# Performance work log

Hardware: AMD Instinct MI355X
Metric: run time of the kernel (lower is better)

The kernel has to match this reference:

```python
import jax, jax.numpy as jnp
import numpy as np

D = 1024
H = 16
DH = D // H


def setup_inputs() -> dict:
    key = jax.random.key(0)
    ks = jax.random.split(key, 7)
    s = 0.02
    return {
        "z": jax.random.normal(ks[0], (8, 1024, D), dtype=jnp.float32),
        "ln_w": jnp.ones((D,), dtype=jnp.float32),
        "ln_b": jnp.zeros((D,), dtype=jnp.float32),
        "W_qkv": jax.random.normal(ks[1], (D, 3 * D), dtype=jnp.float32) * s,
        "b_qkv": jnp.zeros((3 * D,), dtype=jnp.float32),
        "W_proj": jax.random.normal(ks[2], (D, D), dtype=jnp.float32) * s,
        "b_proj": jnp.zeros((D,), dtype=jnp.float32),
    }


def reference(z, ln_w, ln_b, W_qkv, b_qkv, W_proj, b_proj):
    b, n, d = z.shape
    # Pre-LN
    mu = jnp.mean(z, axis=-1, keepdims=True)
    var = jnp.var(z, axis=-1, keepdims=True)
    zn = (z - mu) / jnp.sqrt(var + 1e-5) * ln_w + ln_b
    # QKV projection: [b, n, 3, H, DH]
    qkv = (zn @ W_qkv + b_qkv).reshape(b, n, 3, H, DH)
    q = qkv[:, :, 0].transpose(0, 2, 1, 3)  # [b, H, n, DH]
    k = qkv[:, :, 1].transpose(0, 2, 1, 3)
    v = qkv[:, :, 2].transpose(0, 2, 1, 3)
    scale = 1.0 / jnp.sqrt(jnp.asarray(DH, dtype=z.dtype))
    scores = jnp.einsum("bhqd,bhkd->bhqk", q, k) * scale
    attn = jax.nn.softmax(scores, axis=-1)
    msa = jnp.einsum("bhqk,bhkd->bhqd", attn, v)  # [b, H, n, DH]
    msa_cat = msa.transpose(0, 2, 1, 3).reshape(b, n, d)
    out = msa_cat @ W_proj + b_proj
    return z + out
```

## Files before the change

kernel.cpp:

```cpp
#include <hip/hip_runtime.h>
#include <stdint.h>

typedef unsigned short u16;
typedef uint8_t u8;
typedef __bf16 bf16x8 __attribute__((ext_vector_type(8)));
typedef float f32x4 __attribute__((ext_vector_type(4)));
typedef int i32x8 __attribute__((ext_vector_type(8)));

#define D_MODEL 1024
#define NHEADS  16
#define DHEAD   64
#define BATCH   8
#define SEQ     1024
#define MTOT    (BATCH*SEQ)

#define GPTR(p) ((const __attribute__((address_space(1))) void*)(p))
#define LPTR(p) ((__attribute__((address_space(3))) void*)(p))

#if defined(__HIP_DEVICE_COMPILE__)
  #define MFMA_FP8_16x16x128(a, b, c) \
      __builtin_amdgcn_mfma_scale_f32_16x16x128_f8f6f4((a), (b), (c), 0, 0, 0, 127, 0, 127)
  #define CVT_PK_FP8(a, b, old, w) __builtin_amdgcn_cvt_pk_fp8_f32((a), (b), (old), (w))
#else
  #define MFMA_FP8_16x16x128(a, b, c) (c)
  #define CVT_PK_FP8(a, b, old, w) (0)
#endif

__device__ __forceinline__ u16 f2bf(float f) {
    union { float f; uint32_t u; } v; v.f = f;
    uint32_t u = v.u;
    u += 0x7fffu + ((u >> 16) & 1u);
    return (u16)(u >> 16);
}

__device__ __forceinline__ uint32_t pklo(int i1, int i0) {
    return __builtin_amdgcn_perm((uint32_t)i1, (uint32_t)i0, 0x05040100u);
}

__global__ __launch_bounds__(256) void prep_inputs(
    const float* __restrict__ z, const float* __restrict__ w,
    const float* __restrict__ b, uint32_t* __restrict__ znf,
    const float* __restrict__ Wqkv, const float* __restrict__ Wproj,
    u8* __restrict__ outQkv, u8* __restrict__ outProj)
{
    __shared__ float red[8];
    __shared__ u8 tile[32][36];
    const int bid = blockIdx.x;
    const int t = threadIdx.x;
    if (bid < MTOT) {
        const int row = bid;
        const float4 v = reinterpret_cast<const float4*>(z + (size_t)row * D_MODEL)[t];
        float s  = v.x + v.y + v.z + v.w;
        float s2 = v.x*v.x + v.y*v.y + v.z*v.z + v.w*v.w;
        #pragma unroll
        for (int off = 32; off; off >>= 1) {
            s  += __shfl_down(s,  off, 64);
            s2 += __shfl_down(s2, off, 64);
        }
        const int wave = t >> 6, lane = t & 63;
        if (lane == 0) { red[wave] = s; red[wave + 4] = s2; }
        __syncthreads();
        if (t == 0) {
            float ts  = red[0] + red[1] + red[2] + red[3];
            float ts2 = red[4] + red[5] + red[6] + red[7];
            float mu  = ts * (1.0f / D_MODEL);
            float var = ts2 * (1.0f / D_MODEL) - mu * mu;
            red[0] = mu; red[1] = rsqrtf(var + 1e-5f);
        }
        __syncthreads();
        const float mu = red[0], rstd = red[1];
        const float4 wv = reinterpret_cast<const float4*>(w)[t];
        const float4 bv = reinterpret_cast<const float4*>(b)[t];
        const float x0 = (v.x - mu) * rstd * wv.x + bv.x;
        const float x1 = (v.y - mu) * rstd * wv.y + bv.y;
        const float x2 = (v.z - mu) * rstd * wv.z + bv.z;
        const float x3 = (v.w - mu) * rstd * wv.w + bv.w;
        int pk = CVT_PK_FP8(x0, x1, 0, false);
        pk = CVT_PK_FP8(x2, x3, pk, true);
        znf[(size_t)row * (D_MODEL / 4) + t] = (uint32_t)pk;
    } else {
        const int bx = bid - MTOT;
        const int cx = bx & 127;
        const int r0 = (bx >> 7) * 32;
        const float* in; u8* out; int C;
        if (cx < 96) { in = Wqkv;  out = outQkv;  C = 3072; }
        else         { in = Wproj; out = outProj; C = 1024; }
        const int c0 = (cx < 96 ? cx : cx - 96) * 32;
        const int tx = t & 31, ty = t >> 5;
        #pragma unroll
        for (int i = 0; i < 4; ++i) {
            const float f = in[(size_t)(r0 + ty + i*8) * C + c0 + tx];
            tile[ty + i*8][tx] = (u8)(CVT_PK_FP8(f, 0.f, 0, false) & 0xFF);
        }
        __syncthreads();
        #pragma unroll
        for (int i = 0; i < 4; ++i)
            out[(size_t)(c0 + ty + i*8) * D_MODEL + r0 + tx] = tile[tx][ty + i*8];
    }
}

#define QSCALE 23.0831207f

#define FP8_MAINLOOP(A_, Bt_, MFMA_STMT)                                        \
    __shared__ u8 As[128 * 128];                                                \
    __shared__ u8 Bs[128 * 128];                                                \
    const int tid = threadIdx.x;                                                \
    const int wave = tid >> 6, lane = tid & 63;                                 \
    const int lm = lane & 15, g = lane >> 4;                                    \
    const int wm = (wave >> 1) * 64, wn = (wave & 1) * 64;                      \
    const int m0 = blockIdx.y * 128, n0 = blockIdx.x * 128;                     \
    const int srow = tid >> 3;                                                  \
    const int sseg = tid & 7;                                                   \
    const int sgcol = (sseg ^ (srow & 7)) * 16;                                 \
    const int xl = lm & 7;                                                      \
    const int ca0 = ((2 * g) ^ xl) * 16;                                        \
    const int ca1 = ((2 * g + 1) ^ xl) * 16;                                    \
    f32x4 acc[4][4] = {};                                                       \
    for (int k0 = 0; k0 < D_MODEL; k0 += 128) {                                 \
        _Pragma("unroll")                                                       \
        for (int c = 0; c < 4; ++c) {                                           \
            const int r = srow + c * 32;                                        \
            __builtin_amdgcn_global_load_lds(                                   \
                GPTR(&A_[(size_t)(m0 + r) * D_MODEL + k0 + sgcol]),             \
                LPTR(&As[r * 128 + sseg * 16]), 16, 0, 0);                      \
            __builtin_amdgcn_global_load_lds(                                   \
                GPTR(&Bt_[(size_t)(n0 + r) * D_MODEL + k0 + sgcol]),            \
                LPTR(&Bs[r * 128 + sseg * 16]), 16, 0, 0);                      \
        }                                                                       \
        __syncthreads();                                                        \
        i32x8 af[4], bfr[4];                                                    \
        _Pragma("unroll")                                                       \
        for (int i = 0; i < 4; ++i) {                                           \
            const uint4 alo = *reinterpret_cast<const uint4*>(&As[(wm + i*16 + lm) * 128 + ca0]); \
            const uint4 ahi = *reinterpret_cast<const uint4*>(&As[(wm + i*16 + lm) * 128 + ca1]); \
            af[i][0] = alo.x; af[i][1] = alo.y; af[i][2] = alo.z; af[i][3] = alo.w; \
            af[i][4] = ahi.x; af[i][5] = ahi.y; af[i][6] = ahi.z; af[i][7] = ahi.w; \
            const uint4 blo = *reinterpret_cast<const uint4*>(&Bs[(wn + i*16 + lm) * 128 + ca0]); \
            const uint4 bhi = *reinterpret_cast<const uint4*>(&Bs[(wn + i*16 + lm) * 128 + ca1]); \
            bfr[i][0] = blo.x; bfr[i][1] = blo.y; bfr[i][2] = blo.z; bfr[i][3] = blo.w; \
            bfr[i][4] = bhi.x; bfr[i][5] = bhi.y; bfr[i][6] = bhi.z; bfr[i][7] = bhi.w; \
        }                                                                       \
        _Pragma("unroll")                                                       \
        for (int i = 0; i < 4; ++i)                                             \
            _Pragma("unroll")                                                   \
            for (int j = 0; j < 4; ++j)                                         \
                MFMA_STMT;                                                      \
        __syncthreads();                                                        \
    }

__global__ __launch_bounds__(256, 2) void gemm_qk(
    const u8* __restrict__ A, const u8* __restrict__ Bt,
    const float* __restrict__ bias,
    u16* __restrict__ q, u16* __restrict__ k)
{
    FP8_MAINLOOP(A, Bt, acc[i][j] = MFMA_FP8_16x16x128(bfr[j], af[i], acc[i][j]))
    const int colbase = n0 + wn;
    const int sel = colbase >> 10;
    const int h = (colbase & 1023) >> 6;
    u16* dst = (sel == 0) ? q : k;
    const float scl = (sel == 0) ? QSCALE : 1.0f;
    #pragma unroll
    for (int j = 0; j < 4; ++j) {
        const int dh0 = j * 16 + 4 * g;
        const float4 bv4 = *reinterpret_cast<const float4*>(&bias[colbase + dh0]);
        #pragma unroll
        for (int i = 0; i < 4; ++i) {
            const int m = m0 + wm + i * 16 + lm;
            const int b = m >> 10, t = m & 1023;
            ushort4 o;
            o.x = f2bf((acc[i][j][0] + bv4.x) * scl);
            o.y = f2bf((acc[i][j][1] + bv4.y) * scl);
            o.z = f2bf((acc[i][j][2] + bv4.z) * scl);
            o.w = f2bf((acc[i][j][3] + bv4.w) * scl);
            *reinterpret_cast<ushort4*>(
                &dst[(((size_t)(b * NHEADS + h)) * SEQ + t) * DHEAD + dh0]) = o;
        }
    }
}

__global__ __launch_bounds__(256, 2) void gemm_v(
    const u8* __restrict__ A, const u8* __restrict__ Btv,
    const float* __restrict__ biasv, u16* __restrict__ vT)
{
    FP8_MAINLOOP(A, Btv, acc[i][j] = MFMA_FP8_16x16x128(af[i], bfr[j], acc[i][j]))
    const int colbase = n0 + wn;
    const int h = colbase >> 6;
    #pragma unroll
    for (int j = 0; j < 4; ++j) {
        const int dh = ((colbase & 63) + j * 16) + lm;
        const float bv = biasv[colbase + j * 16 + lm];
        #pragma unroll
        for (int i = 0; i < 4; ++i) {
            const int t0 = m0 + wm + i * 16 + 4 * g;
            const int b = t0 >> 10, t = t0 & 1023;
            ushort4 o;
            o.x = f2bf(acc[i][j][0] + bv);
            o.y = f2bf(acc[i][j][1] + bv);
            o.z = f2bf(acc[i][j][2] + bv);
            o.w = f2bf(acc[i][j][3] + bv);
            *reinterpret_cast<ushort4*>(
                &vT[(((size_t)(b * NHEADS + h)) * DHEAD + dh) * SEQ + t]) = o;
        }
    }
}

__global__ __launch_bounds__(256, 2) void gemm_proj(
    const u8* __restrict__ A, const u8* __restrict__ Bt,
    const float* __restrict__ bias, const float* __restrict__ z,
    float* __restrict__ out)
{
    FP8_MAINLOOP(A, Bt, acc[i][j] = MFMA_FP8_16x16x128(bfr[j], af[i], acc[i][j]))
    #pragma unroll
    for (int j = 0; j < 4; ++j) {
        const int col0 = n0 + wn + j * 16 + 4 * g;
        const float4 bv4 = *reinterpret_cast<const float4*>(&bias[col0]);
        #pragma unroll
        for (int i = 0; i < 4; ++i) {
            const int m = m0 + wm + i * 16 + lm;
            const size_t idx = (size_t)m * D_MODEL + col0;
            const float4 zv = *reinterpret_cast<const float4*>(&z[idx]);
            float4 ov;
            ov.x = zv.x + acc[i][j][0] + bv4.x;
            ov.y = zv.y + acc[i][j][1] + bv4.y;
            ov.z = zv.z + acc[i][j][2] + bv4.z;
            ov.w = zv.w + acc[i][j][3] + bv4.w;
            *reinterpret_cast<float4*>(&out[idx]) = ov;
        }
    }
}

#define KLD 68
#define EXP2_MAGIC 12582912.0f

__global__ __launch_bounds__(256, 4) void attn_kernel(
    const u16* __restrict__ Q, const u16* __restrict__ K,
    const u16* __restrict__ Vt, u8* __restrict__ msaf)
{
    __shared__ u16 Ks[64 * KLD];
    __shared__ u16 Vs[64 * KLD];
    const int tid = threadIdx.x, wave = tid >> 6, lane = tid & 63;
    const int lm = lane & 15, g = lane >> 4;
    const int bi = blockIdx.x;
    const int bh = bi & 127;
    const int q0 = (bi >> 7) * 128;
    const int b = bh >> 4, h = bh & 15;
    const size_t headBase = (size_t)bh * SEQ * DHEAD;
    const u16* Qh = Q + headBase;
    const u16* Kh = K + headBase;
    const u16* Vh = Vt + headBase;

    const int srow = tid >> 3, sseg = tid & 7;
    const int aA = 16 * (sseg >> 2) + 4 * (sseg & 3);

    const uint4 onesu = {0x3F803F80u, 0x3F803F80u, 0x3F803F80u, 0x3F803F80u};
    const bf16x8 ONES = __builtin_bit_cast(bf16x8, onesu);
    const f32x4 SMINIT = {16250.0f, 16250.0f, 16250.0f, 16250.0f};

    bf16x8 qf[2][2];
    #pragma unroll
    for (int s = 0; s < 2; ++s) {
        const u16* qrow = Qh + (size_t)(q0 + s * 64 + wave * 16 + lm) * DHEAD;
        qf[s][0] = *reinterpret_cast<const bf16x8*>(qrow + g * 8);
        qf[s][1] = *reinterpret_cast<const bf16x8*>(qrow + 32 + g * 8);
    }

    f32x4 o[2][4] = {};
    f32x4 lacc[2] = {};

    for (int j0 = 0; j0 < SEQ; j0 += 64) {
        #pragma unroll
        for (int s2 = 0; s2 < 2; ++s2) {
            const int row = srow + 32 * s2;
            *reinterpret_cast<uint4*>(&Ks[row * KLD + sseg * 8]) =
                *reinterpret_cast<const uint4*>(&Kh[(size_t)(j0 + row) * DHEAD + sseg * 8]);
            const u16* vrow = Vh + (size_t)row * SEQ + j0;
            const uint2 va = *reinterpret_cast<const uint2*>(vrow + aA);
            const uint2 vb = *reinterpret_cast<const uint2*>(vrow + 32 + aA);
            uint4 wv; wv.x = va.x; wv.y = va.y; wv.z = vb.x; wv.w = vb.y;
            *reinterpret_cast<uint4*>(&Vs[row * KLD + sseg * 8]) = wv;
        }
        __syncthreads();

        bf16x8 kf0[4], kf1[4];
        #pragma unroll
        for (int ni = 0; ni < 4; ++ni) {
            kf0[ni] = *reinterpret_cast<const bf16x8*>(&Ks[(ni*16 + lm) * KLD + g * 8]);
            kf1[ni] = *reinterpret_cast<const bf16x8*>(&Ks[(ni*16 + lm) * KLD + 32 + g * 8]);
        }

        bf16x8 pfr[2][2];
        #pragma unroll
        for (int s = 0; s < 2; ++s) {
            f32x4 st[4];
            __builtin_amdgcn_s_setprio(1);
            #pragma unroll
            for (int ni = 0; ni < 4; ++ni) {
                st[ni] = __builtin_amdgcn_mfma_f32_16x16x32_bf16(kf0[ni], qf[s][0], SMINIT, 0, 0, 0);
                st[ni] = __builtin_amdgcn_mfma_f32_16x16x32_bf16(kf1[ni], qf[s][1], st[ni], 0, 0, 0);
            }
            __builtin_amdgcn_s_setprio(0);
            int ip[4][4];
            #pragma unroll
            for (int ni = 0; ni < 4; ++ni)
                #pragma unroll
                for (int r = 0; r < 4; ++r)
                    ip[ni][r] = __builtin_bit_cast(int, st[ni][r] + EXP2_MAGIC);
            #pragma unroll
            for (int c = 0; c < 2; ++c) {
                uint4 u;
                u.x = pklo(ip[c][1],   ip[c][0]);
                u.y = pklo(ip[c][3],   ip[c][2]);
                u.z = pklo(ip[c+2][1], ip[c+2][0]);
                u.w = pklo(ip[c+2][3], ip[c+2][2]);
                pfr[s][c] = __builtin_bit_cast(bf16x8, u);
            }
            lacc[s] = __builtin_amdgcn_mfma_f32_16x16x32_bf16(ONES, pfr[s][0], lacc[s], 0, 0, 0);
            lacc[s] = __builtin_amdgcn_mfma_f32_16x16x32_bf16(ONES, pfr[s][1], lacc[s], 0, 0, 0);
        }

        __builtin_amdgcn_s_setprio(1);
        #pragma unroll
        for (int mt = 0; mt < 4; ++mt) {
            bf16x8 vf0 = *reinterpret_cast<const bf16x8*>(&Vs[(mt*16 + lm) * KLD + g * 8]);
            bf16x8 vf1 = *reinterpret_cast<const bf16x8*>(&Vs[(mt*16 + lm) * KLD + 32 + g * 8]);
            #pragma unroll
            for (int s = 0; s < 2; ++s) {
                o[s][mt] = __builtin_amdgcn_mfma_f32_16x16x32_bf16(vf0, pfr[s][0], o[s][mt], 0, 0, 0);
                o[s][mt] = __builtin_amdgcn_mfma_f32_16x16x32_bf16(vf1, pfr[s][1], o[s][mt], 0, 0, 0);
            }
        }
        __builtin_amdgcn_s_setprio(0);
        __syncthreads();
    }

    #pragma unroll
    for (int s = 0; s < 2; ++s) {
        const float inv = 1.0f / lacc[s][0];
        const int t = q0 + s * 64 + wave * 16 + lm;
        const size_t base = ((size_t)b * SEQ + t) * D_MODEL + h * DHEAD;
        #pragma unroll
        for (int mt = 0; mt < 4; ++mt) {
            const int d0 = mt * 16 + 4 * g;
            int pk = CVT_PK_FP8(o[s][mt][0] * inv, o[s][mt][1] * inv, 0, false);
            pk = CVT_PK_FP8(o[s][mt][2] * inv, o[s][mt][3] * inv, pk, true);
            *reinterpret_cast<uint32_t*>(&msaf[base + d0]) = (uint32_t)pk;
        }
    }
}

extern "C" void kernel_launch(void* const* d_in, const int* in_sizes, int n_in,
                              void* d_out, int out_size, void* d_ws, size_t ws_size,
                              hipStream_t stream) {
    const float* z      = (const float*)d_in[0];
    const float* ln_w   = (const float*)d_in[1];
    const float* ln_b   = (const float*)d_in[2];
    const float* W_qkv  = (const float*)d_in[3];
    const float* b_qkv  = (const float*)d_in[4];
    const float* W_proj = (const float*)d_in[5];
    const float* b_proj = (const float*)d_in[6];
    float* out = (float*)d_out;

    u8* ws = (u8*)d_ws;
    u8*  znf     = ws;
    u8*  wqkvTf  = znf + (size_t)MTOT * D_MODEL;
    u8*  wprojTf = wqkvTf + (size_t)3 * D_MODEL * D_MODEL;
    u8*  msaf    = wprojTf + (size_t)D_MODEL * D_MODEL;
    u16* q       = (u16*)(msaf + (size_t)MTOT * D_MODEL);
    u16* k       = q + (size_t)MTOT * D_MODEL;
    u16* vT      = k + (size_t)MTOT * D_MODEL;

    prep_inputs<<<MTOT + 4096, 256, 0, stream>>>(
        z, ln_w, ln_b, (uint32_t*)znf, W_qkv, W_proj, wqkvTf, wprojTf);
    gemm_qk<<<dim3(16, MTOT / 128), 256, 0, stream>>>(znf, wqkvTf, b_qkv, q, k);
    gemm_v<<<dim3(8, MTOT / 128), 256, 0, stream>>>(
        znf, wqkvTf + (size_t)2048 * D_MODEL, b_qkv + 2048, vT);
    attn_kernel<<<BATCH * NHEADS * (SEQ / 128), 256, 0, stream>>>(q, k, vT, msaf);
    gemm_proj<<<dim3(D_MODEL / 128, MTOT / 128), 256, 0, stream>>>(
        msaf, wprojTf, b_proj, z, out);
}
```

Measured before the change: 205.2 us.

## Double-buffer K/V tiles in attention with register prefetch

The attention loop now prefetches the next K/V tile into registers at the start of each iteration, computes on the current LDS buffer, then writes the prefetched data into the alternate LDS buffer. This drops one __syncthreads per iteration and hides global-load latency behind the MFMA work. In exchange LDS use per block doubles and register pressure rises, which may cut occupancy under launch_bounds(256,4). The final iteration issues a redundant wrap-around load of tile 0.

```diff
diff --git a/kernel.cpp b/kernel.cpp
--- a/kernel.cpp
+++ b/kernel.cpp
@@ -230,14 +230,15 @@
 }
 
 #define KLD 68
+#define TILE_HALF (64 * KLD)
 #define EXP2_MAGIC 12582912.0f
 
 __global__ __launch_bounds__(256, 4) void attn_kernel(
     const u16* __restrict__ Q, const u16* __restrict__ K,
     const u16* __restrict__ Vt, u8* __restrict__ msaf)
 {
-    __shared__ u16 Ks[64 * KLD];
-    __shared__ u16 Vs[64 * KLD];
+    __shared__ u16 Ks[2 * TILE_HALF];
+    __shared__ u16 Vs[2 * TILE_HALF];
     const int tid = threadIdx.x, wave = tid >> 6, lane = tid & 63;
     const int lm = lane & 15, g = lane >> 4;
     const int bi = blockIdx.x;
@@ -264,28 +265,44 @@
         qf[s][1] = *reinterpret_cast<const bf16x8*>(qrow + 32 + g * 8);
     }
 
+    uint4 kr[2], vr[2];
+    #define STAGE_LOAD(jj)                                                      \
+        _Pragma("unroll")                                                       \
+        for (int s2 = 0; s2 < 2; ++s2) {                                        \
+            const int row = srow + 32 * s2;                                     \
+            kr[s2] = *reinterpret_cast<const uint4*>(                           \
+                &Kh[(size_t)((jj) + row) * DHEAD + sseg * 8]);                  \
+            const u16* vrow = Vh + (size_t)row * SEQ + (jj);                    \
+            const uint2 va = *reinterpret_cast<const uint2*>(vrow + aA);        \
+            const uint2 vb = *reinterpret_cast<const uint2*>(vrow + 32 + aA);   \
+            vr[s2].x = va.x; vr[s2].y = va.y; vr[s2].z = vb.x; vr[s2].w = vb.y; \
+        }
+    #define STAGE_WRITE(bo_)                                                    \
+        _Pragma("unroll")                                                       \
+        for (int s2 = 0; s2 < 2; ++s2) {                                        \
+            const int row = srow + 32 * s2;                                     \
+            *reinterpret_cast<uint4*>(&Ks[(bo_) + row * KLD + sseg * 8]) = kr[s2]; \
+            *reinterpret_cast<uint4*>(&Vs[(bo_) + row * KLD + sseg * 8]) = vr[s2]; \
+        }
+
     f32x4 o[2][4] = {};
     f32x4 lacc[2] = {};
 
-    for (int j0 = 0; j0 < SEQ; j0 += 64) {
-        #pragma unroll
-        for (int s2 = 0; s2 < 2; ++s2) {
-            const int row = srow + 32 * s2;
-            *reinterpret_cast<uint4*>(&Ks[row * KLD + sseg * 8]) =
-                *reinterpret_cast<const uint4*>(&Kh[(size_t)(j0 + row) * DHEAD + sseg * 8]);
-            const u16* vrow = Vh + (size_t)row * SEQ + j0;
-            const uint2 va = *reinterpret_cast<const uint2*>(vrow + aA);
-            const uint2 vb = *reinterpret_cast<const uint2*>(vrow + 32 + aA);
-            uint4 wv; wv.x = va.x; wv.y = va.y; wv.z = vb.x; wv.w = vb.y;
-            *reinterpret_cast<uint4*>(&Vs[row * KLD + sseg * 8]) = wv;
-        }
+    STAGE_LOAD(0)
+    STAGE_WRITE(0)
+    int cur = 0;
+
+    for (int it = 0; it < SEQ / 64; ++it) {
+        const int jn = ((it + 1) & (SEQ / 64 - 1)) * 64;
+        STAGE_LOAD(jn)
         __syncthreads();
+        const int bo = cur * TILE_HALF;
 
         bf16x8 kf0[4], kf1[4];
         #pragma unroll
         for (int ni = 0; ni < 4; ++ni) {
-            kf0[ni] = *reinterpret_cast<const bf16x8*>(&Ks[(ni*16 + lm) * KLD + g * 8]);
-            kf1[ni] = *reinterpret_cast<const bf16x8*>(&Ks[(ni*16 + lm) * KLD + 32 + g * 8]);
+            kf0[ni] = *reinterpret_cast<const bf16x8*>(&Ks[bo + (ni*16 + lm) * KLD + g * 8]);
+            kf1[ni] = *reinterpret_cast<const bf16x8*>(&Ks[bo + (ni*16 + lm) * KLD + 32 + g * 8]);
         }
 
         bf16x8 pfr[2][2];
@@ -321,8 +338,8 @@
         __builtin_amdgcn_s_setprio(1);
         #pragma unroll
         for (int mt = 0; mt < 4; ++mt) {
-            bf16x8 vf0 = *reinterpret_cast<const bf16x8*>(&Vs[(mt*16 + lm) * KLD + g * 8]);
-            bf16x8 vf1 = *reinterpret_cast<const bf16x8*>(&Vs[(mt*16 + lm) * KLD + 32 + g * 8]);
+            bf16x8 vf0 = *reinterpret_cast<const bf16x8*>(&Vs[bo + (mt*16 + lm) * KLD + g * 8]);
+            bf16x8 vf1 = *reinterpret_cast<const bf16x8*>(&Vs[bo + (mt*16 + lm) * KLD + 32 + g * 8]);
             #pragma unroll
             for (int s = 0; s < 2; ++s) {
                 o[s][mt] = __builtin_amdgcn_mfma_f32_16x16x32_bf16(vf0, pfr[s][0], o[s][mt], 0, 0, 0);
@@ -330,7 +347,9 @@
             }
         }
         __builtin_amdgcn_s_setprio(0);
-        __syncthreads();
+
+        STAGE_WRITE((cur ^ 1) * TILE_HALF)
+        cur ^= 1;
     }
 
     #pragma unroll
```

Result: slower. 282.1 us (+37.5%).

## Double-buffer FP8 GEMM mainloop LDS tiles to overlap loads with MFMA

Applied to the files above, without the earlier changes.

The shared FP8 GEMM mainloop now keeps two LDS buffers for the A and B tiles. A prologue loads the first K-tile, and each iteration issues the global-to-LDS loads for the next tile before reading the current one and running the MFMAs. The barrier that used to follow the loads is removed, so only the barrier at the end of each iteration remains. This is meant to hide global load latency behind compute. In exchange, LDS use per block doubles to 64KB, which may limit how many blocks fit on a CU.

```diff
diff --git a/kernel.cpp b/kernel.cpp
--- a/kernel.cpp
+++ b/kernel.cpp
@@ -102,8 +102,8 @@
 #define QSCALE 23.0831207f
 
 #define FP8_MAINLOOP(A_, Bt_, MFMA_STMT)                                        \
-    __shared__ u8 As[128 * 128];                                                \
-    __shared__ u8 Bs[128 * 128];                                                \
+    __shared__ u8 As[2][128 * 128];                                             \
+    __shared__ u8 Bs[2][128 * 128];                                             \
     const int tid = threadIdx.x;                                                \
     const int wave = tid >> 6, lane = tid & 63;                                 \
     const int lm = lane & 15, g = lane >> 4;                                    \
@@ -116,27 +116,41 @@
     const int ca0 = ((2 * g) ^ xl) * 16;                                        \
     const int ca1 = ((2 * g + 1) ^ xl) * 16;                                    \
     f32x4 acc[4][4] = {};                                                       \
+    _Pragma("unroll")                                                           \
+    for (int c = 0; c < 4; ++c) {                                               \
+        const int r = srow + c * 32;                                            \
+        __builtin_amdgcn_global_load_lds(                                       \
+            GPTR(&A_[(size_t)(m0 + r) * D_MODEL + sgcol]),                      \
+            LPTR(&As[0][r * 128 + sseg * 16]), 16, 0, 0);                       \
+        __builtin_amdgcn_global_load_lds(                                       \
+            GPTR(&Bt_[(size_t)(n0 + r) * D_MODEL + sgcol]),                     \
+            LPTR(&Bs[0][r * 128 + sseg * 16]), 16, 0, 0);                       \
+    }                                                                           \
+    __syncthreads();                                                            \
+    _Pragma("unroll 2")                                                         \
     for (int k0 = 0; k0 < D_MODEL; k0 += 128) {                                 \
-        _Pragma("unroll")                                                       \
-        for (int c = 0; c < 4; ++c) {                                           \
-            const int r = srow + c * 32;                                        \
-            __builtin_amdgcn_global_load_lds(                                   \
-                GPTR(&A_[(size_t)(m0 + r) * D_MODEL + k0 + sgcol]),             \
-                LPTR(&As[r * 128 + sseg * 16]), 16, 0, 0);                      \
-            __builtin_amdgcn_global_load_lds(                                   \
-                GPTR(&Bt_[(size_t)(n0 + r) * D_MODEL + k0 + sgcol]),            \
-                LPTR(&Bs[r * 128 + sseg * 16]), 16, 0, 0);                      \
+        const int cur = (k0 >> 7) & 1;                                          \
+        if (k0 + 128 < D_MODEL) {                                               \
+            _Pragma("unroll")                                                   \
+            for (int c = 0; c < 4; ++c) {                                       \
+                const int r = srow + c * 32;                                    \
+                __builtin_amdgcn_global_load_lds(                               \
+                    GPTR(&A_[(size_t)(m0 + r) * D_MODEL + k0 + 128 + sgcol]),   \
+                    LPTR(&As[cur ^ 1][r * 128 + sseg * 16]), 16, 0, 0);         \
+                __builtin_amdgcn_global_load_lds(                               \
+                    GPTR(&Bt_[(size_t)(n0 + r) * D_MODEL + k0 + 128 + sgcol]),  \
+                    LPTR(&Bs[cur ^ 1][r * 128 + sseg * 16]), 16, 0, 0);         \
+            }                                                                   \
         }                                                                       \
-        __syncthreads();                                                        \
         i32x8 af[4], bfr[4];                                                    \
         _Pragma("unroll")                                                       \
         for (int i = 0; i < 4; ++i) {                                           \
-            const uint4 alo = *reinterpret_cast<const uint4*>(&As[(wm + i*16 + lm) * 128 + ca0]); \
-            const uint4 ahi = *reinterpret_cast<const uint4*>(&As[(wm + i*16 + lm) * 128 + ca1]); \
+            const uint4 alo = *reinterpret_cast<const uint4*>(&As[cur][(wm + i*16 + lm) * 128 + ca0]); \
+            const uint4 ahi = *reinterpret_cast<const uint4*>(&As[cur][(wm + i*16 + lm) * 128 + ca1]); \
             af[i][0] = alo.x; af[i][1] = alo.y; af[i][2] = alo.z; af[i][3] = alo.w; \
             af[i][4] = ahi.x; af[i][5] = ahi.y; af[i][6] = ahi.z; af[i][7] = ahi.w; \
-            const uint4 blo = *reinterpret_cast<const uint4*>(&Bs[(wn + i*16 + lm) * 128 + ca0]); \
-            const uint4 bhi = *reinterpret_cast<const uint4*>(&Bs[(wn + i*16 + lm) * 128 + ca1]); \
+            const uint4 blo = *reinterpret_cast<const uint4*>(&Bs[cur][(wn + i*16 + lm) * 128 + ca0]); \
+            const uint4 bhi = *reinterpret_cast<const uint4*>(&Bs[cur][(wn + i*16 + lm) * 128 + ca1]); \
             bfr[i][0] = blo.x; bfr[i][1] = blo.y; bfr[i][2] = blo.z; bfr[i][3] = blo.w; \
             bfr[i][4] = bhi.x; bfr[i][5] = bhi.y; bfr[i][6] = bhi.z; bfr[i][7] = bhi.w; \
         }                                                                       \
```

Result: no change. 208.5 us (+1.6%).

## Merge QK and V GEMM launches; process two K/V tiles per attention barrier

Applied to the files above, without the earlier changes.

Combines the separate QK and V projection GEMMs into one launch whose blocks branch on blockIdx.x, so one dispatch covers all 24 column tiles and a launch plus tail wave are removed. The attention kernel now stages two 64-key K/V tiles into doubled shared buffers per iteration, halving the number of barrier pairs per key sweep. The cost is doubled attention LDS usage, which may lower occupancy, and a merged GEMM with branch-dependent epilogues that could raise register pressure.

```diff
diff --git a/kernel.cpp b/kernel.cpp
--- a/kernel.cpp
+++ b/kernel.cpp
@@ -101,20 +101,20 @@
 
 #define QSCALE 23.0831207f
 
-#define FP8_MAINLOOP(A_, Bt_, MFMA_STMT)                                        \
-    __shared__ u8 As[128 * 128];                                                \
-    __shared__ u8 Bs[128 * 128];                                                \
+#define GEMM_PRELUDE                                                            \
     const int tid = threadIdx.x;                                                \
     const int wave = tid >> 6, lane = tid & 63;                                 \
     const int lm = lane & 15, g = lane >> 4;                                    \
     const int wm = (wave >> 1) * 64, wn = (wave & 1) * 64;                      \
-    const int m0 = blockIdx.y * 128, n0 = blockIdx.x * 128;                     \
+    const int m0 = blockIdx.y * 128;                                            \
     const int srow = tid >> 3;                                                  \
     const int sseg = tid & 7;                                                   \
     const int sgcol = (sseg ^ (srow & 7)) * 16;                                 \
     const int xl = lm & 7;                                                      \
     const int ca0 = ((2 * g) ^ xl) * 16;                                        \
-    const int ca1 = ((2 * g + 1) ^ xl) * 16;                                    \
+    const int ca1 = ((2 * g + 1) ^ xl) * 16;
+
+#define FP8_KLOOP(As_, Bs_, A_, Bt_, n0_, MFMA_STMT)                            \
     f32x4 acc[4][4] = {};                                                       \
     for (int k0 = 0; k0 < D_MODEL; k0 += 128) {                                 \
         _Pragma("unroll")                                                       \
@@ -122,21 +122,21 @@
             const int r = srow + c * 32;                                        \
             __builtin_amdgcn_global_load_lds(                                   \
                 GPTR(&A_[(size_t)(m0 + r) * D_MODEL + k0 + sgcol]),             \
-                LPTR(&As[r * 128 + sseg * 16]), 16, 0, 0);                      \
+                LPTR(&As_[r * 128 + sseg * 16]), 16, 0, 0);                     \
             __builtin_amdgcn_global_load_lds(                                   \
-                GPTR(&Bt_[(size_t)(n0 + r) * D_MODEL + k0 + sgcol]),            \
-                LPTR(&Bs[r * 128 + sseg * 16]), 16, 0, 0);                      \
+                GPTR(&Bt_[(size_t)((n0_) + r) * D_MODEL + k0 + sgcol]),         \
+                LPTR(&Bs_[r * 128 + sseg * 16]), 16, 0, 0);                     \
         }                                                                       \
         __syncthreads();                                                        \
         i32x8 af[4], bfr[4];                                                    \
         _Pragma("unroll")                                                       \
         for (int i = 0; i < 4; ++i) {                                           \
-            const uint4 alo = *reinterpret_cast<const uint4*>(&As[(wm + i*16 + lm) * 128 + ca0]); \
-            const uint4 ahi = *reinterpret_cast<const uint4*>(&As[(wm + i*16 + lm) * 128 + ca1]); \
+            const uint4 alo = *reinterpret_cast<const uint4*>(&As_[(wm + i*16 + lm) * 128 + ca0]); \
+            const uint4 ahi = *reinterpret_cast<const uint4*>(&As_[(wm + i*16 + lm) * 128 + ca1]); \
             af[i][0] = alo.x; af[i][1] = alo.y; af[i][2] = alo.z; af[i][3] = alo.w; \
             af[i][4] = ahi.x; af[i][5] = ahi.y; af[i][6] = ahi.z; af[i][7] = ahi.w; \
-            const uint4 blo = *reinterpret_cast<const uint4*>(&Bs[(wn + i*16 + lm) * 128 + ca0]); \
-            const uint4 bhi = *reinterpret_cast<const uint4*>(&Bs[(wn + i*16 + lm) * 128 + ca1]); \
+            const uint4 blo = *reinterpret_cast<const uint4*>(&Bs_[(wn + i*16 + lm) * 128 + ca0]); \
+            const uint4 bhi = *reinterpret_cast<const uint4*>(&Bs_[(wn + i*16 + lm) * 128 + ca1]); \
             bfr[i][0] = blo.x; bfr[i][1] = blo.y; bfr[i][2] = blo.z; bfr[i][3] = blo.w; \
             bfr[i][4] = bhi.x; bfr[i][5] = bhi.y; bfr[i][6] = bhi.z; bfr[i][7] = bhi.w; \
         }                                                                       \
@@ -148,58 +148,61 @@
         __syncthreads();                                                        \
     }
 
-__global__ __launch_bounds__(256, 2) void gemm_qk(
+__global__ __launch_bounds__(256, 2) void gemm_qkv(
     const u8* __restrict__ A, const u8* __restrict__ Bt,
     const float* __restrict__ bias,
-    u16* __restrict__ q, u16* __restrict__ k)
+    u16* __restrict__ q, u16* __restrict__ k, u16* __restrict__ vT)
 {
-    FP8_MAINLOOP(A, Bt, acc[i][j] = MFMA_FP8_16x16x128(bfr[j], af[i], acc[i][j]))
-    const int colbase = n0 + wn;
-    const int sel = colbase >> 10;
-    const int h = (colbase & 1023) >> 6;
-    u16* dst = (sel == 0) ? q : k;
-    const float scl = (sel == 0) ? QSCALE : 1.0f;
-    #pragma unroll
-    for (int j = 0; j < 4; ++j) {
-        const int dh0 = j * 16 + 4 * g;
-        const float4 bv4 = *reinterpret_cast<const float4*>(&bias[colbase + dh0]);
-        #pragma unroll
-        for (int i = 0; i < 4; ++i) {
-            const int m = m0 + wm + i * 16 + lm;
-            const int b = m >> 10, t = m & 1023;
-            ushort4 o;
-            o.x = f2bf((acc[i][j][0] + bv4.x) * scl);
-            o.y = f2bf((acc[i][j][1] + bv4.y) * scl);
-            o.z = f2bf((acc[i][j][2] + bv4.z) * scl);
-            o.w = f2bf((acc[i][j][3] + bv4.w) * scl);
-            *reinterpret_cast<ushort4*>(
-                &dst[(((size_t)(b * NHEADS + h)) * SEQ + t) * DHEAD + dh0]) = o;
-        }
-    }
-}
-
-__global__ __launch_bounds__(256, 2) void gemm_v(
-    const u8* __restrict__ A, const u8* __restrict__ Btv,
-    const float* __restrict__ biasv, u16* __restrict__ vT)
-{
-    FP8_MAINLOOP(A, Btv, acc[i][j] = MFMA_FP8_16x16x128(af[i], bfr[j], acc[i][j]))
-    const int colbase = n0 + wn;
-    const int h = colbase >> 6;
-    #pragma unroll
-    for (int j = 0; j < 4; ++j) {
-        const int dh = ((colbase & 63) + j * 16) + lm;
-        const float bv = biasv[colbase + j * 16 + lm];
-        #pragma unroll
-        for (int i = 0; i < 4; ++i) {
-            const int t0 = m0 + wm + i * 16 + 4 * g;
-            const int b = t0 >> 10, t = t0 & 1023;
-            ushort4 o;
-            o.x = f2bf(acc[i][j][0] + bv);
-            o.y = f2bf(acc[i][j][1] + bv);
-            o.z = f2bf(acc[i][j][2] + bv);
-            o.w = f2bf(acc[i][j][3] + bv);
-            *reinterpret_cast<ushort4*>(
-                &vT[(((size_t)(b * NHEADS + h)) * DHEAD + dh) * SEQ + t]) = o;
+    __shared__ u8 As[128 * 128];
+    __shared__ u8 Bs[128 * 128];
+    GEMM_PRELUDE
+    const int bx = blockIdx.x;
+    if (bx < 16) {
+        const int n0 = bx * 128;
+        FP8_KLOOP(As, Bs, A, Bt, n0, acc[i][j] = MFMA_FP8_16x16x128(bfr[j], af[i], acc[i][j]))
+        const int colbase = n0 + wn;
+        const int sel = colbase >> 10;
+        const int h = (colbase & 1023) >> 6;
+        u16* dst = (sel == 0) ? q : k;
+        const float scl = (sel == 0) ? QSCALE : 1.0f;
+        #pragma unroll
+        for (int j = 0; j < 4; ++j) {
+            const int dh0 = j * 16 + 4 * g;
+            const float4 bv4 = *reinterpret_cast<const float4*>(&bias[colbase + dh0]);
+            #pragma unroll
+            for (int i = 0; i < 4; ++i) {
+                const int m = m0 + wm + i * 16 + lm;
+                const int b = m >> 10, t = m & 1023;
+                ushort4 o;
+                o.x = f2bf((acc[i][j][0] + bv4.x) * scl);
+                o.y = f2bf((acc[i][j][1] + bv4.y) * scl);
+                o.z = f2bf((acc[i][j][2] + bv4.z) * scl);
+                o.w = f2bf((acc[i][j][3] + bv4.w) * scl);
+                *reinterpret_cast<ushort4*>(
+                    &dst[(((size_t)(b * NHEADS + h)) * SEQ + t) * DHEAD + dh0]) = o;
+            }
+        }
+    } else {
+        const int n0 = 2048 + (bx - 16) * 128;
+        FP8_KLOOP(As, Bs, A, Bt, n0, acc[i][j] = MFMA_FP8_16x16x128(af[i], bfr[j], acc[i][j]))
+        const int vcol = (n0 - 2048) + wn;
+        const int h = vcol >> 6;
+        #pragma unroll
+        for (int j = 0; j < 4; ++j) {
+            const int dh = ((vcol & 63) + j * 16) + lm;
+            const float bv = bias[2048 + vcol + j * 16 + lm];
+            #pragma unroll
+            for (int i = 0; i < 4; ++i) {
+                const int t0 = m0 + wm + i * 16 + 4 * g;
+                const int b = t0 >> 10, t = t0 & 1023;
+                ushort4 o;
+                o.x = f2bf(acc[i][j][0] + bv);
+                o.y = f2bf(acc[i][j][1] + bv);
+                o.z = f2bf(acc[i][j][2] + bv);
+                o.w = f2bf(acc[i][j][3] + bv);
+                *reinterpret_cast<ushort4*>(
+                    &vT[(((size_t)(b * NHEADS + h)) * DHEAD + dh) * SEQ + t]) = o;
+            }
         }
     }
 }
@@ -209,7 +212,11 @@
     const float* __restrict__ bias, const float* __restrict__ z,
     float* __restrict__ out)
 {
-    FP8_MAINLOOP(A, Bt, acc[i][j] = MFMA_FP8_16x16x128(bfr[j], af[i], acc[i][j]))
+    __shared__ u8 As[128 * 128];
+    __shared__ u8 Bs[128 * 128];
+    GEMM_PRELUDE
+    const int n0 = blockIdx.x * 128;
+    FP8_KLOOP(As, Bs, A, Bt, n0, acc[i][j] = MFMA_FP8_16x16x128(bfr[j], af[i], acc[i][j]))
     #pragma unroll
     for (int j = 0; j < 4; ++j) {
         const int col0 = n0 + wn + j * 16 + 4 * g;
@@ -236,8 +243,8 @@
     const u16* __restrict__ Q, const u16* __restrict__ K,
     const u16* __restrict__ Vt, u8* __restrict__ msaf)
 {
-    __shared__ u16 Ks[64 * KLD];
-    __shared__ u16 Vs[64 * KLD];
+    __shared__ u16 Ks[2][64 * KLD];
+    __shared__ u16 Vs[2][64 * KLD];
     const int tid = threadIdx.x, wave = tid >> 6, lane = tid & 63;
     const int lm = lane & 15, g = lane >> 4;
     const int bi = blockIdx.x;
@@ -267,69 +274,76 @@
     f32x4 o[2][4] = {};
     f32x4 lacc[2] = {};
 
-    for (int j0 = 0; j0 < SEQ; j0 += 64) {
-        #pragma unroll
-        for (int s2 = 0; s2 < 2; ++s2) {
-            const int row = srow + 32 * s2;
-            *reinterpret_cast<uint4*>(&Ks[row * KLD + sseg * 8]) =
-                *reinterpret_cast<const uint4*>(&Kh[(size_t)(j0 + row) * DHEAD + sseg * 8]);
-            const u16* vrow = Vh + (size_t)row * SEQ + j0;
-            const uint2 va = *reinterpret_cast<const uint2*>(vrow + aA);
-            const uint2 vb = *reinterpret_cast<const uint2*>(vrow + 32 + aA);
-            uint4 wv; wv.x = va.x; wv.y = va.y; wv.z = vb.x; wv.w = vb.y;
-            *reinterpret_cast<uint4*>(&Vs[row * KLD + sseg * 8]) = wv;
-        }
-        __syncthreads();
-
-        bf16x8 kf0[4], kf1[4];
-        #pragma unroll
-        for (int ni = 0; ni < 4; ++ni) {
-            kf0[ni] = *reinterpret_cast<const bf16x8*>(&Ks[(ni*16 + lm) * KLD + g * 8]);
-            kf1[ni] = *reinterpret_cast<const bf16x8*>(&Ks[(ni*16 + lm) * KLD + 32 + g * 8]);
-        }
-
-        bf16x8 pfr[2][2];
-        #pragma unroll
-        for (int s = 0; s < 2; ++s) {
-            f32x4 st[4];
+    for (int j0 = 0; j0 < SEQ; j0 += 128) {
+        #pragma unroll
+        for (int hb = 0; hb < 2; ++hb) {
+            const int jj = j0 + hb * 64;
+            #pragma unroll
+            for (int s2 = 0; s2 < 2; ++s2) {
+                const int row = srow + 32 * s2;
+                *reinterpret_cast<uint4*>(&Ks[hb][row * KLD + sseg * 8]) =
+                    *reinterpret_cast<const uint4*>(&Kh[(size_t)(jj + row) * DHEAD + sseg * 8]);
+                const u16* vrow = Vh + (size_t)row * SEQ + jj;
+                const uint2 va = *reinterpret_cast<const uint2*>(vrow + aA);
+                const uint2 vb = *reinterpret_cast<const uint2*>(vrow + 32 + aA);
+                uint4 wv; wv.x = va.x; wv.y = va.y; wv.z = vb.x; wv.w = vb.y;
+                *reinterpret_cast<uint4*>(&Vs[hb][row * KLD + sseg * 8]) = wv;
+            }
+        }
+        __syncthreads();
+
+        #pragma unroll
+        for (int hb = 0; hb < 2; ++hb) {
+            bf16x8 kf0[4], kf1[4];
+            #pragma unroll
+            for (int ni = 0; ni < 4; ++ni) {
+                kf0[ni] = *reinterpret_cast<const bf16x8*>(&Ks[hb][(ni*16 + lm) * KLD + g * 8]);
+                kf1[ni] = *reinterpret_cast<const bf16x8*>(&Ks[hb][(ni*16 + lm) * KLD + 32 + g * 8]);
+            }
+
+            bf16x8 pfr[2][2];
+            #pragma unroll
+            for (int s = 0; s < 2; ++s) {
+                f32x4 st[4];
+                __builtin_amdgcn_s_setprio(1);
+                #pragma unroll
+                for (int ni = 0; ni < 4; ++ni) {
+                    st[ni] = __builtin_amdgcn_mfma_f32_16x16x32_bf16(kf0[ni], qf[s][0], SMINIT, 0, 0, 0);
+                    st[ni] = __builtin_amdgcn_mfma_f32_16x16x32_bf16(kf1[ni], qf[s][1], st[ni], 0, 0, 0);
+                }
+                __builtin_amdgcn_s_setprio(0);
+                int ip[4][4];
+                #pragma unroll
+                for (int ni = 0; ni < 4; ++ni)
+                    #pragma unroll
+                    for (int r = 0; r < 4; ++r)
+                        ip[ni][r] = __builtin_bit_cast(int, st[ni][r] + EXP2_MAGIC);
+                #pragma unroll
+                for (int c = 0; c < 2; ++c) {
+                    uint4 u;
+                    u.x = pklo(ip[c][1],   ip[c][0]);
+                    u.y = pklo(ip[c][3],   ip[c][2]);
+                    u.z = pklo(ip[c+2][1], ip[c+2][0]);
+                    u.w = pklo(ip[c+2][3], ip[c+2][2]);
+                    pfr[s][c] = __builtin_bit_cast(bf16x8, u);
+                }
+                lacc[s] = __builtin_amdgcn_mfma_f32_16x16x32_bf16(ONES, pfr[s][0], lacc[s], 0, 0, 0);
+                lacc[s] = __builtin_amdgcn_mfma_f32_16x16x32_bf16(ONES, pfr[s][1], lacc[s], 0, 0, 0);
+            }
+
             __builtin_amdgcn_s_setprio(1);
             #pragma unroll
-            for (int ni = 0; ni < 4; ++ni) {
-                st[ni] = __builtin_amdgcn_mfma_f32_16x16x32_bf16(kf0[ni], qf[s][0], SMINIT, 0, 0, 0);
-                st[ni] = __builtin_amdgcn_mfma_f32_16x16x32_bf16(kf1[ni], qf[s][1], st[ni], 0, 0, 0);
+            for (int mt = 0; mt < 4; ++mt) {
+                bf16x8 vf0 = *reinterpret_cast<const bf16x8*>(&Vs[hb][(mt*16 + lm) * KLD + g * 8]);
+                bf16x8 vf1 = *reinterpret_cast<const bf16x8*>(&Vs[hb][(mt*16 + lm) * KLD + 32 + g * 8]);
+                #pragma unroll
+                for (int s = 0; s < 2; ++s) {
+                    o[s][mt] = __builtin_amdgcn_mfma_f32_16x16x32_bf16(vf0, pfr[s][0], o[s][mt], 0, 0, 0);
+                    o[s][mt] = __builtin_amdgcn_mfma_f32_16x16x32_bf16(vf1, pfr[s][1], o[s][mt], 0, 0, 0);
+                }
             }
             __builtin_amdgcn_s_setprio(0);
-            int ip[4][4];
-            #pragma unroll
-            for (int ni = 0; ni < 4; ++ni)
-                #pragma unroll
-                for (int r = 0; r < 4; ++r)
-                    ip[ni][r] = __builtin_bit_cast(int, st[ni][r] + EXP2_MAGIC);
-            #pragma unroll
-            for (int c = 0; c < 2; ++c) {
-                uint4 u;
-                u.x = pklo(ip[c][1],   ip[c][0]);
-                u.y = pklo(ip[c][3],   ip[c][2]);
-                u.z = pklo(ip[c+2][1], ip[c+2][0]);
-                u.w = pklo(ip[c+2][3], ip[c+2][2]);
-                pfr[s][c] = __builtin_bit_cast(bf16x8, u);
-            }
-            lacc[s] = __builtin_amdgcn_mfma_f32_16x16x32_bf16(ONES, pfr[s][0], lacc[s], 0, 0, 0);
-            lacc[s] = __builtin_amdgcn_mfma_f32_16x16x32_bf16(ONES, pfr[s][1], lacc[s], 0, 0, 0);
-        }
-
-        __builtin_amdgcn_s_setprio(1);
-        #pragma unroll
-        for (int mt = 0; mt < 4; ++mt) {
-            bf16x8 vf0 = *reinterpret_cast<const bf16x8*>(&Vs[(mt*16 + lm) * KLD + g * 8]);
-            bf16x8 vf1 = *reinterpret_cast<const bf16x8*>(&Vs[(mt*16 + lm) * KLD + 32 + g * 8]);
-            #pragma unroll
-            for (int s = 0; s < 2; ++s) {
-                o[s][mt] = __builtin_amdgcn_mfma_f32_16x16x32_bf16(vf0, pfr[s][0], o[s][mt], 0, 0, 0);
-                o[s][mt] = __builtin_amdgcn_mfma_f32_16x16x32_bf16(vf1, pfr[s][1], o[s][mt], 0, 0, 0);
-            }
-        }
-        __builtin_amdgcn_s_setprio(0);
+        }
         __syncthreads();
     }
 
@@ -371,9 +385,7 @@
 
     prep_inputs<<<MTOT + 4096, 256, 0, stream>>>(
         z, ln_w, ln_b, (uint32_t*)znf, W_qkv, W_proj, wqkvTf, wprojTf);
-    gemm_qk<<<dim3(16, MTOT / 128), 256, 0, stream>>>(znf, wqkvTf, b_qkv, q, k);
-    gemm_v<<<dim3(8, MTOT / 128), 256, 0, stream>>>(
-        znf, wqkvTf + (size_t)2048 * D_MODEL, b_qkv + 2048, vT);
+    gemm_qkv<<<dim3(24, MTOT / 128), 256, 0, stream>>>(znf, wqkvTf, b_qkv, q, k, vT);
     attn_kernel<<<BATCH * NHEADS * (SEQ / 128), 256, 0, stream>>>(q, k, vT, msaf);
     gemm_proj<<<dim3(D_MODEL / 128, MTOT / 128), 256, 0, stream>>>(
         msaf, wprojTf, b_proj, z, out);
```

After: 206.3 us. No clear change (+0.5%).
